# Performance work log

Measured on AMD Instinct MI355X. Metric: run time of the kernel, lower is better.

Reference implementation:

```python
import jax, jax.numpy as jnp
import numpy as np

N_EMB = 4096
EMB_DIM = 256
BETA = 10.0


def setup_inputs() -> dict:
    key = jax.random.key(0)
    k1, k2 = jax.random.split(key)
    z = jax.random.normal(k1, (32, EMB_DIM, 32, 32), dtype=jnp.float32)
    # matches nn.Embedding init: uniform(-1/n_embeddings, 1/n_embeddings)
    embedding = jax.random.uniform(
        k2, (N_EMB, EMB_DIM), dtype=jnp.float32,
        minval=-1.0 / N_EMB, maxval=1.0 / N_EMB)
    return {"z": z, "embedding": embedding}


def reference(z, embedding):
    sg = jax.lax.stop_gradient
    # NCHW -> NHWC
    zp = jnp.transpose(z, (0, 2, 3, 1))  # [B,H,W,D]
    zf = zp.reshape(-1, EMB_DIM)         # [N,D]
    # squared distances: ||z||^2 + ||e||^2 - 2 z.e^T
    d = (jnp.sum(zf * zf, axis=1, keepdims=True)
         + jnp.sum(embedding * embedding, axis=1)
         - 2.0 * jnp.matmul(zf, embedding.T))  # [N,K]
    min_encoding_indices = jnp.argmin(d, axis=1)  # [N]
    z_q = embedding[min_encoding_indices].reshape(zp.shape)  # [B,H,W,D]
    loss = (jnp.mean((sg(z_q) - zp) ** 2)
            + BETA * jnp.mean((z_q - sg(zp)) ** 2))
    # straight-through estimator
    z_q_ste = zp + sg(z_q - zp)
    z_q_out = jnp.transpose(z_q_ste, (0, 3, 1, 2))  # back to NCHW
    return (z_q_out, loss, min_encoding_indices)
```

## Files before the change

kernel.cpp:

```cpp
#include <hip/hip_runtime.h>

#define DIM   256
#define HW_   1024
#define NROWS 32768
#define KEMB  4096

#define WS_S_OFF    131072
#define WS_E_OFF    262144
#define WS_LOSS_OFF 278528
#define WS_DONE_OFF 278536
#define WS_CNT_OFF  278592
#define WS_CAND_OFF 540736
#define WS_EBUF_OFF 1589312
#define WS_NEEDED   3686464
#define RESCUE_W    1.5e-4f

typedef __attribute__((ext_vector_type(8))) short bf16x8;
typedef __attribute__((ext_vector_type(4))) float f32x4;

__device__ __forceinline__ unsigned short f2bf(float v) {
  unsigned u = __float_as_uint(v);
  return (unsigned short)((u + 0x7FFFu + ((u >> 16) & 1u)) >> 16);
}

__device__ __forceinline__ float np_sumsq_128(const float* q, int stride) {
#pragma clang fp contract(off)
  float r[8];
#pragma unroll
  for (int i = 0; i < 8; ++i) { float v = q[i * stride]; r[i] = v * v; }
  for (int blk = 8; blk < 128; blk += 8) {
#pragma unroll
    for (int i = 0; i < 8; ++i) {
      float v = q[(blk + i) * stride];
      float sq = v * v;
      r[i] = r[i] + sq;
    }
  }
  return ((r[0] + r[1]) + (r[2] + r[3])) + ((r[4] + r[5]) + (r[6] + r[7]));
}

__global__ __launch_bounds__(256) void prep_kernel(
    const float* __restrict__ z, const float* __restrict__ emb,
    float* __restrict__ S, float* __restrict__ E, short* __restrict__ ebuf,
    double* __restrict__ loss_sum, int* __restrict__ done, int do_filter) {
#pragma clang fp contract(off)
  if (blockIdx.x < 144) {
    int t = blockIdx.x * 256 + threadIdx.x;
    if (t == 0) { loss_sum[0] = 0.0; done[0] = 0; }
    if (t < NROWS) {
      if (!do_filter) {
        int b = t >> 10, hw = t & 1023;
        const float* p = z + (size_t)b * (DIM * HW_) + hw;
        float s0 = np_sumsq_128(p, HW_);
        float s1 = np_sumsq_128(p + 128 * HW_, HW_);
        S[t] = s0 + s1;
      }
    } else if (t < NROWS + KEMB) {
      int j = t - NROWS;
      const float* p = emb + (size_t)j * DIM;
      float s0 = np_sumsq_128(p, 1);
      float s1 = np_sumsq_128(p + 128, 1);
      E[j] = s0 + s1;
    }
  } else {
    if (!do_filter) return;
    int u = (blockIdx.x - 144) * 256 + threadIdx.x;
    int lane = u & 63;
    int ks = (u >> 6) & 7;
    int g16 = u >> 9;
    int j = g16 * 16 + (lane & 15);
    int kb = ks * 32 + (lane >> 4) * 8;
    const float* p = emb + (size_t)j * DIM + kb;
    short out[8];
#pragma unroll
    for (int i = 0; i < 8; ++i) out[i] = (short)f2bf(p[i]);
    *(bf16x8*)(ebuf + (size_t)u * 8) = *(bf16x8*)out;
  }
}

__global__ __launch_bounds__(512, 3) void filter2_kernel(
    const float* __restrict__ z, const short* __restrict__ ebuf,
    const float* __restrict__ E, int* __restrict__ cnt_g,
    int* __restrict__ cand_g) {
  __shared__ __align__(16) short Ab[32 * 512];
  __shared__ float rowmin_l[64][8];
  __shared__ float thr_l[64];
  __shared__ int   cnt_l[64];
  __shared__ int   cand_l[64][8];

  const int t = threadIdx.x;
  const int w = t >> 6, lane = t & 63;
  const int quad = lane >> 4, l16 = lane & 15;
  const int nb = blockIdx.x * 64;
  const int b = nb >> 10, hwb = nb & 1023;

  {
    const float* zb2 = z + (size_t)b * (DIM * HW_) + hwb;
    const int k0 = w * 32 + quad * 8;
#pragma unroll
    for (int mt = 0; mt < 4; ++mt) {
      const int r = mt * 16 + l16;
      short tmp[8];
#pragma unroll
      for (int i = 0; i < 8; ++i)
        tmp[i] = (short)f2bf(zb2[(size_t)(k0 + i) * HW_ + r]);
      *(bf16x8*)(Ab + ((mt * 8 + w) * 64 + lane) * 8) = *(bf16x8*)tmp;
    }
  }
  __syncthreads();

  const f32x4 zero = {0.0f, 0.0f, 0.0f, 0.0f};
  const short* Abl = Ab + lane * 8;

  float runmin[4][4];
#pragma unroll
  for (int mt = 0; mt < 4; ++mt)
#pragma unroll
    for (int rg = 0; rg < 4; ++rg) runmin[mt][rg] = 3.0e38f;

#pragma unroll 1
  for (int grp = 0; grp < 8; ++grp) {
    const int jb = w * 512 + grp * 64;
    const int g16b = jb >> 4;
    f32x4 acc[4][4];
#pragma unroll
    for (int jt = 0; jt < 4; ++jt)
#pragma unroll
      for (int mt = 0; mt < 4; ++mt) acc[jt][mt] = zero;
#pragma unroll 1
    for (int ks = 0; ks < 8; ++ks) {
      bf16x8 av[4];
#pragma unroll
      for (int mt = 0; mt < 4; ++mt)
        av[mt] = *(const bf16x8*)(Abl + (mt * 8 + ks) * 512);
#pragma unroll
      for (int jt = 0; jt < 4; ++jt) {
        bf16x8 bfr = *(const bf16x8*)(ebuf +
            ((size_t)(g16b + jt) * 8 + ks) * 512 + lane * 8);
#pragma unroll
        for (int mt = 0; mt < 4; ++mt)
          acc[jt][mt] = __builtin_amdgcn_mfma_f32_16x16x32_bf16(
              av[mt], bfr, acc[jt][mt], 0, 0, 0);
      }
    }
#pragma unroll
    for (int jt = 0; jt < 4; ++jt) {
      float Ej = E[jb + jt * 16 + l16];
#pragma unroll
      for (int mt = 0; mt < 4; ++mt)
#pragma unroll
        for (int rg = 0; rg < 4; ++rg) {
          float g = fmaf(-2.0f, acc[jt][mt][rg], Ej);
          runmin[mt][rg] = fminf(runmin[mt][rg], g);
        }
    }
  }
#pragma unroll
  for (int mt = 0; mt < 4; ++mt)
#pragma unroll
    for (int rg = 0; rg < 4; ++rg) {
      float m = runmin[mt][rg];
#pragma unroll
      for (int mask = 1; mask <= 8; mask <<= 1)
        m = fminf(m, __shfl_xor(m, mask, 64));
      runmin[mt][rg] = m;
    }
  if (l16 == 0) {
#pragma unroll
    for (int mt = 0; mt < 4; ++mt)
#pragma unroll
      for (int rg = 0; rg < 4; ++rg)
        rowmin_l[mt * 16 + quad * 4 + rg][w] = runmin[mt][rg];
  }
  __syncthreads();
  if (t < 64) {
    float m0 = fminf(fminf(rowmin_l[t][0], rowmin_l[t][1]),
                     fminf(rowmin_l[t][2], rowmin_l[t][3]));
    float m1 = fminf(fminf(rowmin_l[t][4], rowmin_l[t][5]),
                     fminf(rowmin_l[t][6], rowmin_l[t][7]));
    thr_l[t] = fminf(m0, m1) + RESCUE_W;
    cnt_l[t] = 0;
  }
  __syncthreads();
  float thrv[4][4];
#pragma unroll
  for (int mt = 0; mt < 4; ++mt)
#pragma unroll
    for (int rg = 0; rg < 4; ++rg)
      thrv[mt][rg] = thr_l[mt * 16 + quad * 4 + rg];

#pragma unroll 1
  for (int grp = 0; grp < 8; ++grp) {
    const int jb = w * 512 + grp * 64;
    const int g16b = jb >> 4;
    f32x4 acc[4][4];
#pragma unroll
    for (int jt = 0; jt < 4; ++jt)
#pragma unroll
      for (int mt = 0; mt < 4; ++mt) acc[jt][mt] = zero;
#pragma unroll 1
    for (int ks = 0; ks < 8; ++ks) {
      bf16x8 av[4];
#pragma unroll
      for (int mt = 0; mt < 4; ++mt)
        av[mt] = *(const bf16x8*)(Abl + (mt * 8 + ks) * 512);
#pragma unroll
      for (int jt = 0; jt < 4; ++jt) {
        bf16x8 bfr = *(const bf16x8*)(ebuf +
            ((size_t)(g16b + jt) * 8 + ks) * 512 + lane * 8);
#pragma unroll
        for (int mt = 0; mt < 4; ++mt)
          acc[jt][mt] = __builtin_amdgcn_mfma_f32_16x16x32_bf16(
              av[mt], bfr, acc[jt][mt], 0, 0, 0);
      }
    }
#pragma unroll
    for (int jt = 0; jt < 4; ++jt) {
      int jcol = jb + jt * 16 + l16;
      float Ej = E[jcol];
#pragma unroll
      for (int mt = 0; mt < 4; ++mt)
#pragma unroll
        for (int rg = 0; rg < 4; ++rg) {
          float g = fmaf(-2.0f, acc[jt][mt][rg], Ej);
          if (g <= thrv[mt][rg]) {
            int rl = mt * 16 + quad * 4 + rg;
            int slot = atomicAdd(&cnt_l[rl], 1);
            if (slot < 8) cand_l[rl][slot] = jcol;
          }
        }
    }
  }
  __syncthreads();
  if (t < 64) {
    int c = cnt_l[t];
    cnt_g[nb + t] = c;
    int cc = c > 8 ? 8 : c;
    for (int p = 0; p < cc; ++p) cand_g[(size_t)(nb + t) * 8 + p] = cand_l[t][p];
  }
}

#define XPAD 257
__global__ __launch_bounds__(256, 2) void exact_cand_kernel(
    const float* __restrict__ z, const float* __restrict__ emb,
    const float* __restrict__ E,
    const int* __restrict__ cnt_g, const int* __restrict__ cand_g,
    int* __restrict__ idx_out, float* __restrict__ idxf_out) {
  __shared__ float z_l[64 * XPAD];
  const int t = threadIdx.x;
  const int nb = blockIdx.x * 64;
  const int b = nb >> 10, hwb = nb & 1023;
  const float* zb = z + (size_t)b * (DIM * HW_) + hwb;
#pragma unroll
  for (int i = 0; i < 16; ++i) {
    int flat = i * 256 + t;
    int d = flat >> 4, r4 = flat & 15;
    float4 v = *(const float4*)(zb + (size_t)d * HW_ + r4 * 4);
    z_l[(r4 * 4 + 0) * XPAD + d] = v.x;
    z_l[(r4 * 4 + 1) * XPAD + d] = v.y;
    z_l[(r4 * 4 + 2) * XPAD + d] = v.z;
    z_l[(r4 * 4 + 3) * XPAD + d] = v.w;
  }
  __syncthreads();
  if (t >= 64) return;

  const int row = nb + t;
  const float* zrow = z_l + t * XPAD;
  float s;
  {
    float s0 = np_sumsq_128(zrow, 1);
    float s1 = np_sumsq_128(zrow + 128, 1);
    s = s0 + s1;
  }
  int c = cnt_g[row];
  float bd = 3.0e38f; int bj = 0x7fffffff;
  if (c <= 8) {
    for (int p = 0; p < c; ++p) {
      int j = cand_g[(size_t)row * 8 + p];
      const float* e = emb + (size_t)j * DIM;
      float acc = 0.0f;
#pragma unroll 8
      for (int k4 = 0; k4 < 64; ++k4) {
        float4 ev = *(const float4*)(e + k4 * 4);
        acc = fmaf(zrow[k4 * 4 + 0], ev.x, acc);
        acc = fmaf(zrow[k4 * 4 + 1], ev.y, acc);
        acc = fmaf(zrow[k4 * 4 + 2], ev.z, acc);
        acc = fmaf(zrow[k4 * 4 + 3], ev.w, acc);
      }
      float d = fmaf(-2.0f, acc, s + E[j]);
      if (d < bd || (d == bd && j < bj)) { bd = d; bj = j; }
    }
  } else {
    for (int j = 0; j < KEMB; ++j) {
      const float* e = emb + (size_t)j * DIM;
      float acc = 0.0f;
      for (int k4 = 0; k4 < 64; ++k4) {
        float4 ev = *(const float4*)(e + k4 * 4);
        acc = fmaf(zrow[k4 * 4 + 0], ev.x, acc);
        acc = fmaf(zrow[k4 * 4 + 1], ev.y, acc);
        acc = fmaf(zrow[k4 * 4 + 2], ev.z, acc);
        acc = fmaf(zrow[k4 * 4 + 3], ev.w, acc);
      }
      float d = fmaf(-2.0f, acc, s + E[j]);
      if (d < bd || (d == bd && j < bj)) { bd = d; bj = j; }
    }
  }
  idx_out[row] = bj;
  idxf_out[row] = (float)bj;
}

#define RT 64
#define JT 256
#define KC 16
__global__ __launch_bounds__(256, 2) void dist_argmin_kernel(
    const float* __restrict__ z, const float* __restrict__ emb,
    const float* __restrict__ S, const float* __restrict__ E,
    int* __restrict__ idx_out, float* __restrict__ idxf_out) {
  __shared__ float zt[DIM * RT];
  __shared__ float et[KC * JT];
  const int t  = threadIdx.x;
  const int g  = t & 31;
  const int tr = t >> 5;
  const int nb = blockIdx.x * RT;
  const int b  = nb >> 10;
  const int hwb = nb & 1023;
  const float* zb = z + (size_t)b * (DIM * HW_) + hwb;
#pragma unroll
  for (int i = 0; i < 16; ++i) {
    int flat = t + i * 256;
    int k  = flat >> 4;
    int r4 = flat & 15;
    float4 v = *(const float4*)(zb + (size_t)k * HW_ + r4 * 4);
    *(float4*)(zt + flat * 4) = v;
  }
  float bestd[8];
  int   bestj[8];
#pragma unroll
  for (int i = 0; i < 8; ++i) { bestd[i] = 3.0e38f; bestj[i] = 0; }
  float Sreg[8];
#pragma unroll
  for (int rr = 0; rr < 8; ++rr) Sreg[rr] = S[nb + tr * 8 + rr];
  float4 pf[4];
#pragma unroll
  for (int q = 0; q < 4; ++q) {
    int cid = q * 256 + t;
    pf[q] = *(const float4*)(emb + (size_t)(cid >> 2) * DIM + (cid & 3) * 4);
  }
  for (int jt = 0; jt < KEMB / JT; ++jt) {
    float acc[8][8];
#pragma unroll
    for (int rr = 0; rr < 8; ++rr)
#pragma unroll
      for (int c = 0; c < 8; ++c) acc[rr][c] = 0.0f;
    for (int kc = 0; kc < DIM / KC; ++kc) {
      __syncthreads();
#pragma unroll
      for (int q = 0; q < 4; ++q) {
        int cid = q * 256 + t;
        int j = cid >> 2, k4 = cid & 3;
        et[(k4 * 4 + 0) * JT + j] = pf[q].x;
        et[(k4 * 4 + 1) * JT + j] = pf[q].y;
        et[(k4 * 4 + 2) * JT + j] = pf[q].z;
        et[(k4 * 4 + 3) * JT + j] = pf[q].w;
      }
      int s = jt * (DIM / KC) + kc + 1;
      if (s < (KEMB / JT) * (DIM / KC)) {
        int njt = s >> 4, nkc = s & 15;
        const float* base = emb + (size_t)njt * JT * DIM + nkc * KC;
#pragma unroll
        for (int q = 0; q < 4; ++q) {
          int cid = q * 256 + t;
          pf[q] = *(const float4*)(base + (size_t)(cid >> 2) * DIM + (cid & 3) * 4);
        }
      }
      __syncthreads();
      const float* ztk = zt + (kc * KC) * RT;
#pragma unroll
      for (int kk = 0; kk < KC; ++kk) {
        float4 z0 = *(const float4*)(ztk + kk * RT + tr * 8);
        float4 z1 = *(const float4*)(ztk + kk * RT + tr * 8 + 4);
        float2 e0 = *(const float2*)(et + kk * JT + g * 2);
        float2 e1 = *(const float2*)(et + kk * JT + 64 + g * 2);
        float2 e2 = *(const float2*)(et + kk * JT + 128 + g * 2);
        float2 e3 = *(const float2*)(et + kk * JT + 192 + g * 2);
        float zr[8] = {z0.x, z0.y, z0.z, z0.w, z1.x, z1.y, z1.z, z1.w};
        float ev[8] = {e0.x, e0.y, e1.x, e1.y, e2.x, e2.y, e3.x, e3.y};
#pragma unroll
        for (int rr = 0; rr < 8; ++rr)
#pragma unroll
          for (int c = 0; c < 8; ++c)
            acc[rr][c] = fmaf(zr[rr], ev[c], acc[rr][c]);
      }
    }
    int jb = jt * JT;
    float Ereg[8];
#pragma unroll
    for (int c = 0; c < 8; ++c)
      Ereg[c] = E[jb + (c >> 1) * 64 + g * 2 + (c & 1)];
#pragma unroll
    for (int rr = 0; rr < 8; ++rr)
#pragma unroll
      for (int c = 0; c < 8; ++c) {
        float A = Sreg[rr] + Ereg[c];
        float d = fmaf(-2.0f, acc[rr][c], A);
        int j = jb + (c >> 1) * 64 + g * 2 + (c & 1);
        if (d < bestd[rr] || (d == bestd[rr] && j < bestj[rr])) {
          bestd[rr] = d; bestj[rr] = j;
        }
      }
  }
  __syncthreads();
  float* rd = et;
  int*   rj = (int*)(et + 2048);
#pragma unroll
  for (int rr = 0; rr < 8; ++rr) {
    rd[(tr * 8 + rr) * 32 + g] = bestd[rr];
    rj[(tr * 8 + rr) * 32 + g] = bestj[rr];
  }
  __syncthreads();
  if (t < RT) {
    float bd = rd[t * 32];
    int   bj = rj[t * 32];
    for (int c = 1; c < 32; ++c) {
      float d2 = rd[t * 32 + c];
      int   j2 = rj[t * 32 + c];
      if (d2 < bd || (d2 == bd && j2 < bj)) { bd = d2; bj = j2; }
    }
    idx_out[nb + t]  = bj;
    idxf_out[nb + t] = (float)bj;
  }
}

#define EPAD 257
__global__ __launch_bounds__(256) void epilogue_kernel(
    const float* __restrict__ z, const float* __restrict__ emb,
    const int* __restrict__ idx, float* __restrict__ out0,
    double* __restrict__ loss_sum, int* __restrict__ done,
    float* __restrict__ out_loss) {
#pragma clang fp contract(off)
  __shared__ float eq[64 * EPAD];
  __shared__ int   iv_l[64];
  __shared__ double wsum[4];
  const int t = threadIdx.x, w = t >> 6, lane = t & 63;
  const int nb = blockIdx.x * 64;
  const int b = nb >> 10, hwb = nb & 1023;

  if (t < 64) iv_l[t] = idx[nb + t];
  __syncthreads();
  const float4* emb4 = (const float4*)emb;
#pragma unroll
  for (int i = 0; i < 16; ++i) {
    int r = w * 16 + i;
    float4 v = emb4[(size_t)iv_l[r] * 64 + lane];
    *(float4*)(eq + r * EPAD + lane * 4) = v;
  }
  __syncthreads();

  double acc = 0.0;
  const float* zb = z + (size_t)b * (DIM * HW_) + hwb;
  float* ob = out0 + (size_t)b * (DIM * HW_) + hwb;
  for (int dc = 0; dc < 64; ++dc) {
    int d = dc * 4 + w;
    float zp = zb[(size_t)d * HW_ + lane];
    float zq = eq[lane * EPAD + d];
    float td = zq - zp;
    ob[(size_t)d * HW_ + lane] = zp + td;
    acc += (double)(td * td);
  }
#pragma unroll
  for (int off = 32; off > 0; off >>= 1) acc += __shfl_down(acc, off, 64);
  if (lane == 0) wsum[w] = acc;
  __syncthreads();
  if (t == 0) {
    double bsum = (wsum[0] + wsum[1]) + (wsum[2] + wsum[3]);
    atomicAdd(loss_sum, bsum);
    __threadfence();
    int prev = atomicAdd(done, 1);
    if (prev == 511) {
      double m = loss_sum[0] / 8388608.0;
      float mf = (float)m;
      float bb = 10.0f * mf;
      out_loss[0] = mf + bb;
    }
  }
}

extern "C" void kernel_launch(void* const* d_in, const int* in_sizes, int n_in,
                              void* d_out, int out_size, void* d_ws, size_t ws_size,
                              hipStream_t stream) {
  const float* z   = (const float*)d_in[0];
  const float* emb = (const float*)d_in[1];
  float* out = (float*)d_out;
  char* ws = (char*)d_ws;
  int*      idx  = (int*)ws;
  float*    S    = (float*)(ws + WS_S_OFF);
  float*    E    = (float*)(ws + WS_E_OFF);
  double*   ls   = (double*)(ws + WS_LOSS_OFF);
  int*      done = (int*)(ws + WS_DONE_OFF);
  int*      cnt  = (int*)(ws + WS_CNT_OFF);
  int*      cand = (int*)(ws + WS_CAND_OFF);
  short*    ebuf = (short*)(ws + WS_EBUF_OFF);

  const int do_filter = (ws_size >= (size_t)WS_NEEDED) ? 1 : 0;

  prep_kernel<<<656, 256, 0, stream>>>(z, emb, S, E, ebuf, ls, done, do_filter);

  if (do_filter) {
    filter2_kernel<<<512, 512, 0, stream>>>(z, ebuf, E, cnt, cand);
    exact_cand_kernel<<<512, 256, 0, stream>>>(z, emb, E, cnt, cand, idx,
                                               out + 8388609);
  } else {
    dist_argmin_kernel<<<NROWS / RT, 256, 0, stream>>>(z, emb, S, E, idx,
                                                       out + 8388609);
  }

  epilogue_kernel<<<512, 256, 0, stream>>>(z, emb, idx, out, ls, done,
                                           out + 8388608);
}
```

Measured before the change: 263.3 us.

## Fuse exact candidate rescoring with epilogue and parallelize candidates across lanes

Merges the exact candidate rescoring kernel and the epilogue into one finish kernel, so z is loaded once and the epilogue launch plus its re-read of z are gone. Each row's up-to-8 candidates are now scored by 8 lanes in parallel and reduced with shuffles, instead of serially by one thread with 192 idle threads. Blocks shrink to 32 rows, giving 1024 blocks. The done-counter threshold is tied to the new block count, and the epilogue's exact numerical semantics must match the old one.

```diff
diff --git a/kernel.cpp b/kernel.cpp
--- a/kernel.cpp
+++ b/kernel.cpp
@@ -240,73 +240,136 @@
   }
 }
 
-#define XPAD 257
-__global__ __launch_bounds__(256, 2) void exact_cand_kernel(
+#define FROWS 32
+#define FPAD 257
+__global__ __launch_bounds__(256, 2) void finish_kernel(
     const float* __restrict__ z, const float* __restrict__ emb,
     const float* __restrict__ E,
     const int* __restrict__ cnt_g, const int* __restrict__ cand_g,
-    int* __restrict__ idx_out, float* __restrict__ idxf_out) {
-  __shared__ float z_l[64 * XPAD];
+    float* __restrict__ out0, double* __restrict__ loss_sum,
+    int* __restrict__ done, float* __restrict__ out_loss,
+    float* __restrict__ idxf_out) {
+#pragma clang fp contract(off)
+  __shared__ float z_l[FROWS * FPAD];
+  __shared__ float eq[FROWS * FPAD];
+  __shared__ int   iv_l[FROWS];
+  __shared__ double wsum[4];
   const int t = threadIdx.x;
-  const int nb = blockIdx.x * 64;
+  const int nb = blockIdx.x * FROWS;
   const int b = nb >> 10, hwb = nb & 1023;
   const float* zb = z + (size_t)b * (DIM * HW_) + hwb;
-#pragma unroll
-  for (int i = 0; i < 16; ++i) {
-    int flat = i * 256 + t;
-    int d = flat >> 4, r4 = flat & 15;
-    float4 v = *(const float4*)(zb + (size_t)d * HW_ + r4 * 4);
-    z_l[(r4 * 4 + 0) * XPAD + d] = v.x;
-    z_l[(r4 * 4 + 1) * XPAD + d] = v.y;
-    z_l[(r4 * 4 + 2) * XPAD + d] = v.z;
-    z_l[(r4 * 4 + 3) * XPAD + d] = v.w;
-  }
-  __syncthreads();
-  if (t >= 64) return;
-
-  const int row = nb + t;
-  const float* zrow = z_l + t * XPAD;
-  float s;
+
+#pragma unroll
+  for (int i = 0; i < 8; ++i) {
+    int f = i * 256 + t;
+    int k = f >> 3, r4 = f & 7;
+    float4 v = *(const float4*)(zb + (size_t)k * HW_ + r4 * 4);
+    z_l[(r4 * 4 + 0) * FPAD + k] = v.x;
+    z_l[(r4 * 4 + 1) * FPAD + k] = v.y;
+    z_l[(r4 * 4 + 2) * FPAD + k] = v.z;
+    z_l[(r4 * 4 + 3) * FPAD + k] = v.w;
+  }
+  __syncthreads();
+
   {
-    float s0 = np_sumsq_128(zrow, 1);
-    float s1 = np_sumsq_128(zrow + 128, 1);
-    s = s0 + s1;
-  }
-  int c = cnt_g[row];
-  float bd = 3.0e38f; int bj = 0x7fffffff;
-  if (c <= 8) {
-    for (int p = 0; p < c; ++p) {
-      int j = cand_g[(size_t)row * 8 + p];
-      const float* e = emb + (size_t)j * DIM;
-      float acc = 0.0f;
+    const int r = t >> 3, p = t & 7;
+    const int row = nb + r;
+    const float* zrow = z_l + r * FPAD;
+    float s;
+    {
+      float s0 = np_sumsq_128(zrow, 1);
+      float s1 = np_sumsq_128(zrow + 128, 1);
+      s = s0 + s1;
+    }
+    int c = cnt_g[row];
+    float bd = 3.0e38f; int bj = 0x7fffffff;
+    if (c <= 8) {
+      if (p < c) {
+        int j = cand_g[(size_t)row * 8 + p];
+        const float* e = emb + (size_t)j * DIM;
+        float acc = 0.0f;
 #pragma unroll 8
-      for (int k4 = 0; k4 < 64; ++k4) {
-        float4 ev = *(const float4*)(e + k4 * 4);
-        acc = fmaf(zrow[k4 * 4 + 0], ev.x, acc);
-        acc = fmaf(zrow[k4 * 4 + 1], ev.y, acc);
-        acc = fmaf(zrow[k4 * 4 + 2], ev.z, acc);
-        acc = fmaf(zrow[k4 * 4 + 3], ev.w, acc);
-      }
-      float d = fmaf(-2.0f, acc, s + E[j]);
-      if (d < bd || (d == bd && j < bj)) { bd = d; bj = j; }
-    }
-  } else {
-    for (int j = 0; j < KEMB; ++j) {
-      const float* e = emb + (size_t)j * DIM;
-      float acc = 0.0f;
-      for (int k4 = 0; k4 < 64; ++k4) {
-        float4 ev = *(const float4*)(e + k4 * 4);
-        acc = fmaf(zrow[k4 * 4 + 0], ev.x, acc);
-        acc = fmaf(zrow[k4 * 4 + 1], ev.y, acc);
-        acc = fmaf(zrow[k4 * 4 + 2], ev.z, acc);
-        acc = fmaf(zrow[k4 * 4 + 3], ev.w, acc);
-      }
-      float d = fmaf(-2.0f, acc, s + E[j]);
-      if (d < bd || (d == bd && j < bj)) { bd = d; bj = j; }
-    }
-  }
-  idx_out[row] = bj;
-  idxf_out[row] = (float)bj;
+        for (int k4 = 0; k4 < 64; ++k4) {
+          float4 ev = *(const float4*)(e + k4 * 4);
+          acc = fmaf(zrow[k4 * 4 + 0], ev.x, acc);
+          acc = fmaf(zrow[k4 * 4 + 1], ev.y, acc);
+          acc = fmaf(zrow[k4 * 4 + 2], ev.z, acc);
+          acc = fmaf(zrow[k4 * 4 + 3], ev.w, acc);
+        }
+        bd = fmaf(-2.0f, acc, s + E[j]);
+        bj = j;
+      }
+    } else if (p == 0) {
+      for (int j = 0; j < KEMB; ++j) {
+        const float* e = emb + (size_t)j * DIM;
+        float acc = 0.0f;
+        for (int k4 = 0; k4 < 64; ++k4) {
+          float4 ev = *(const float4*)(e + k4 * 4);
+          acc = fmaf(zrow[k4 * 4 + 0], ev.x, acc);
+          acc = fmaf(zrow[k4 * 4 + 1], ev.y, acc);
+          acc = fmaf(zrow[k4 * 4 + 2], ev.z, acc);
+          acc = fmaf(zrow[k4 * 4 + 3], ev.w, acc);
+        }
+        float d = fmaf(-2.0f, acc, s + E[j]);
+        if (d < bd || (d == bd && j < bj)) { bd = d; bj = j; }
+      }
+    }
+#pragma unroll
+    for (int m = 1; m <= 4; m <<= 1) {
+      float od = __shfl_xor(bd, m, 64);
+      int   oj = __shfl_xor(bj, m, 64);
+      if (od < bd || (od == bd && oj < bj)) { bd = od; bj = oj; }
+    }
+    if (p == 0) { iv_l[r] = bj; idxf_out[row] = (float)bj; }
+  }
+  __syncthreads();
+
+  {
+    const int w = t >> 6, lane = t & 63;
+    const float4* emb4 = (const float4*)emb;
+#pragma unroll
+    for (int i = 0; i < 8; ++i) {
+      int r = w * 8 + i;
+      float4 v = emb4[(size_t)iv_l[r] * 64 + lane];
+      *(float4*)(eq + r * FPAD + lane * 4) = v;
+    }
+  }
+  __syncthreads();
+
+  double acc = 0.0;
+  {
+    const int r = t & 31, dq = t >> 5;
+    float* ob = out0 + (size_t)b * (DIM * HW_) + hwb + r;
+    const float* zpr = z_l + r * FPAD;
+    const float* zqr = eq + r * FPAD;
+    for (int dc = 0; dc < 32; ++dc) {
+      int d = dc * 8 + dq;
+      float zp = zpr[d];
+      float zq = zqr[d];
+      float td = zq - zp;
+      ob[(size_t)d * HW_] = zp + td;
+      acc += (double)(td * td);
+    }
+  }
+#pragma unroll
+  for (int off = 32; off > 0; off >>= 1) acc += __shfl_down(acc, off, 64);
+  {
+    const int w = t >> 6, lane = t & 63;
+    if (lane == 0) wsum[w] = acc;
+  }
+  __syncthreads();
+  if (t == 0) {
+    double bsum = (wsum[0] + wsum[1]) + (wsum[2] + wsum[3]);
+    atomicAdd(loss_sum, bsum);
+    __threadfence();
+    int prev = atomicAdd(done, 1);
+    if (prev == 1023) {
+      double m = loss_sum[0] / 8388608.0;
+      float mf = (float)m;
+      float bb = 10.0f * mf;
+      out_loss[0] = mf + bb;
+    }
+  }
 }
 
 #define RT 64
@@ -507,13 +570,13 @@
 
   if (do_filter) {
     filter2_kernel<<<512, 512, 0, stream>>>(z, ebuf, E, cnt, cand);
-    exact_cand_kernel<<<512, 256, 0, stream>>>(z, emb, E, cnt, cand, idx,
-                                               out + 8388609);
+    finish_kernel<<<1024, 256, 0, stream>>>(z, emb, E, cnt, cand, out, ls,
+                                            done, out + 8388608,
+                                            out + 8388609);
   } else {
     dist_argmin_kernel<<<NROWS / RT, 256, 0, stream>>>(z, emb, S, E, idx,
                                                        out + 8388609);
-  }
-
-  epilogue_kernel<<<512, 256, 0, stream>>>(z, emb, idx, out, ls, done,
-                                           out + 8388608);
-}
+    epilogue_kernel<<<512, 256, 0, stream>>>(z, emb, idx, out, ls, done,
+                                             out + 8388608);
+  }
+}
```

Measured after the change: 271.7 us. 3.2% more time.
